# Kernel optimization log

Hardware: AMD Instinct MI355X
Metric: run time of the kernel (lower is better)

Reference implementation:

```python
import jax, jax.numpy as jnp
import numpy as np

N, C, T, V, S = 64, 64, 300, 25, 3  # batch, channels, frames, joints, num_subset
EPS_NORM = 1e-4  # L2_norm epsilon from the torch module
EPS_BN = 1e-5    # torch BatchNorm2d default eps


def setup_inputs() -> dict:
    key = jax.random.key(0)
    ks = jax.random.split(key, 6)
    x = jax.random.normal(ks[0], (N, C, T, V), jnp.float32)
    # adaptive adjacency PA: (num_subset, V, V)
    PA = jax.random.normal(ks[1], (S, V, V), jnp.float32)
    # per-subset 1x1 conv: weight (out_c, in_c), bias (out_c,); conv_branch_init scale
    W = jax.random.normal(ks[2], (S, C, C), jnp.float32) * np.sqrt(2.0 / (C * S)).astype(np.float32)
    b = jax.random.normal(ks[3], (S, C), jnp.float32) * 0.01
    # BatchNorm affine params (training-mode batch stats used in forward)
    gamma = 1.0 + 0.1 * jax.random.normal(ks[4], (C,), jnp.float32)
    beta = 0.1 * jax.random.normal(ks[5], (C,), jnp.float32)
    return {"x": x, "PA": PA, "W": W, "b": b, "gamma": gamma, "beta": beta}


def reference(x, PA, W, b, gamma, beta):
    # L2 normalize adjacency along dim=1 (per subset, per column)
    A = PA / (jnp.linalg.norm(PA, axis=1, keepdims=True) + EPS_NORM)  # (S, V, V)
    # sum over subsets of: graph matmul (nctv,vw->nctw) then 1x1 conv (oc contraction)
    y = jnp.einsum('nctv,svw,soc->notw', x, A, W)
    y = y + b.sum(axis=0)[None, :, None, None]
    # BatchNorm2d in training mode: batch stats over (N, T, V) per channel
    mean = y.mean(axis=(0, 2, 3), keepdims=True)
    var = y.var(axis=(0, 2, 3), keepdims=True)  # biased variance
    y = gamma[None, :, None, None] * (y - mean) * jax.lax.rsqrt(var + EPS_BN) + beta[None, :, None, None]
    # residual (in_c == out_c -> down is identity) + ReLU
    return jax.nn.relu(y + x)
```

## Files before the change

### kernel.cpp

```cpp
#include <hip/hip_runtime.h>
#include <math.h>


typedef __attribute__((ext_vector_type(8))) short bf16x8;
typedef __attribute__((ext_vector_type(4))) float f32x4;
typedef __attribute__((ext_vector_type(4))) ushort u16x4;

__device__ inline ushort f2bf(float f) {
    union { float f; unsigned u; } v; v.f = f;
    unsigned r = v.u + 0x7fffu + ((v.u >> 16) & 1u);
    return (ushort)(r >> 16);
}
__device__ inline float bf2f(ushort h) {
    union { unsigned u; float f; } v; v.u = ((unsigned)h) << 16;
    return v.f;
}

__global__ __launch_bounds__(256) void k_prep(const float* __restrict__ PA,
                                              const float* __restrict__ W,
                                              float* __restrict__ ws) {
    __shared__ float Al[1875];
    const int tid = threadIdx.x;
    const int bid = blockIdx.x;
    for (int i = tid; i < 1875; i += 256) Al[i] = PA[i];
    if (bid == 0)
        for (int i = tid; i < 2048; i += 256) ws[2048 + i] = 0.0f;
    __syncthreads();
    if (tid < 75) {
        int s = tid / 25, w = tid - s * 25;
        float ss = 0.0f;
        for (int v = 0; v < 25; ++v) {
            float p = Al[s * 625 + v * 25 + w];
            ss += p * p;
        }
        float inv = 1.0f / (sqrtf(ss) + 1e-4f);
        for (int v = 0; v < 25; ++v) Al[s * 625 + v * 25 + w] *= inv;
    }
    __syncthreads();
    int idx = bid * 256 + tid;
    if (idx < 1536) {
        ushort* wt = (ushort*)(ws + 4352);
        int lane = idx & 63, rest = idx >> 6;
        int wv = rest & 3, sk = rest >> 2;
        int kt = sk & 1, s = sk >> 1;
        int col = lane & 15, quad = lane >> 4;
        const float* wp = W + s * 4096 + (wv * 16 + col) * 64 + kt * 32 + quad * 8;
#pragma unroll
        for (int j = 0; j < 8; ++j) wt[idx * 8 + j] = f2bf(wp[j]);
    } else if (idx < 1920) {
        ushort* at = (ushort*)(ws + 10496);
        int a = idx - 1536;
        int lane = a & 63, rest = a >> 6;
        int nt2 = rest & 1, s = rest >> 1;
        int col = lane & 15, quad = lane >> 4;
        int w = nt2 * 16 + col;
#pragma unroll
        for (int j = 0; j < 8; ++j) {
            int v = quad * 8 + j;
            float av = (v < 25 && w < 25) ? Al[s * 625 + v * 25 + w] : 0.0f;
            at[a * 8 + j] = f2bf(av);
        }
    }
}

__global__ __launch_bounds__(256, 4) void k_main8(const float* __restrict__ x,
                                                  const float* __restrict__ ws,
                                                  ushort* __restrict__ ypre,
                                                  float* __restrict__ stats) {
    __shared__ __align__(16) ushort Xl[112 * 72];
    __shared__ float sst[128];

    const int tid = threadIdx.x;
    const int wv = tid >> 6;
    const int lane = tid & 63;
    const int col = lane & 15;
    const int quad = lane >> 4;
    const int strip = wv << 4;
    const int n = blockIdx.y;
    const int t0 = blockIdx.x * 4;

    {
        const float* xr = x + n * 480000 + t0 * 25;
        const int c = tid >> 2, part = tid & 3;
        const float4* row = (const float4*)(xr + c * 7500);
        for (int j = part; j < 25; j += 4) {
            float4 v4 = row[j];
            ushort* dst = &Xl[(j * 4) * 72 + c];
            dst[0]   = f2bf(v4.x);
            dst[72]  = f2bf(v4.y);
            dst[144] = f2bf(v4.z);
            dst[216] = f2bf(v4.w);
        }
        for (int i = tid; i < 864; i += 256) Xl[7200 + i] = 0;
    }
    __syncthreads();

    const ushort* wt = (const ushort*)(ws + 4352);
    const ushort* at = (const ushort*)(ws + 10496);

    const int s0l = col + ((quad & 1) << 5);
    const int s1l = s0l + 16;
    const bool hiq = quad >= 2;

    f32x4 yacc[4][2];
#pragma unroll
    for (int t = 0; t < 4; ++t)
#pragma unroll
        for (int j = 0; j < 2; ++j) yacc[t][j] = (f32x4){0.f, 0.f, 0.f, 0.f};

    for (int s = 0; s < 3; ++s) {
        bf16x8 wf0 = *(const bf16x8*)&wt[(((s * 2 + 0) * 4 + wv) * 64 + lane) * 8];
        bf16x8 wf1 = *(const bf16x8*)&wt[(((s * 2 + 1) * 4 + wv) * 64 + lane) * 8];
        bf16x8 af0 = *(const bf16x8*)&at[((s * 2 + 0) * 64 + lane) * 8];
        bf16x8 af1 = *(const bf16x8*)&at[((s * 2 + 1) * 64 + lane) * 8];
#pragma unroll
        for (int t = 0; t < 4; ++t) {
            const int r0 = (t * 25 + col) * 72 + (quad << 3);
            const int r1 = r0 + 16 * 72;
            bf16x8 x00 = *(const bf16x8*)&Xl[r0];
            bf16x8 x01 = *(const bf16x8*)&Xl[r0 + 32];
            bf16x8 x10 = *(const bf16x8*)&Xl[r1];
            bf16x8 x11 = *(const bf16x8*)&Xl[r1 + 32];
            f32x4 zA = (f32x4){0.f, 0.f, 0.f, 0.f};
            f32x4 zB = (f32x4){0.f, 0.f, 0.f, 0.f};
            zA = __builtin_amdgcn_mfma_f32_16x16x32_bf16(x00, wf0, zA, 0, 0, 0);
            zA = __builtin_amdgcn_mfma_f32_16x16x32_bf16(x01, wf1, zA, 0, 0, 0);
            zB = __builtin_amdgcn_mfma_f32_16x16x32_bf16(x10, wf0, zB, 0, 0, 0);
            zB = __builtin_amdgcn_mfma_f32_16x16x32_bf16(x11, wf1, zB, 0, 0, 0);
            unsigned pa0 = (unsigned)f2bf(zA[0]) | ((unsigned)f2bf(zA[1]) << 16);
            unsigned pa1 = (unsigned)f2bf(zA[2]) | ((unsigned)f2bf(zA[3]) << 16);
            unsigned pb0 = (unsigned)f2bf(zB[0]) | ((unsigned)f2bf(zB[1]) << 16);
            unsigned pb1 = (unsigned)f2bf(zB[2]) | ((unsigned)f2bf(zB[3]) << 16);
            unsigned ga0 = __shfl(pa0, s0l);
            unsigned ga1 = __shfl(pa1, s0l);
            unsigned ga2 = __shfl(pa0, s1l);
            unsigned ga3 = __shfl(pa1, s1l);
            unsigned gb0 = __shfl(pb0, s0l);
            unsigned gb1 = __shfl(pb1, s0l);
            unsigned gb2 = __shfl(pb0, s1l);
            unsigned gb3 = __shfl(pb1, s1l);
            union { unsigned u[4]; bf16x8 v; } zf;
            zf.u[0] = hiq ? gb0 : ga0;
            zf.u[1] = hiq ? gb1 : ga1;
            zf.u[2] = hiq ? gb2 : ga2;
            zf.u[3] = hiq ? gb3 : ga3;
            yacc[t][0] = __builtin_amdgcn_mfma_f32_16x16x32_bf16(zf.v, af0, yacc[t][0], 0, 0, 0);
            yacc[t][1] = __builtin_amdgcn_mfma_f32_16x16x32_bf16(zf.v, af1, yacc[t][1], 0, 0, 0);
        }
    }

    float ssum[4] = {0.f, 0.f, 0.f, 0.f}, ssq[4] = {0.f, 0.f, 0.f, 0.f};
    const int obase = strip + (quad << 2);
#pragma unroll
    for (int t = 0; t < 4; ++t)
#pragma unroll
        for (int nt2 = 0; nt2 < 2; ++nt2) {
            int w = nt2 * 16 + col;
            if (w < 25) {
                ushort* yp = ypre + n * 480000 + obase * 7500 + (t0 + t) * 25 + w;
                f32x4 f = yacc[t][nt2];
#pragma unroll
                for (int r = 0; r < 4; ++r) {
                    float yv = f[r];
                    yp[r * 7500] = f2bf(yv);
                    ssum[r] += yv;
                    ssq[r] = fmaf(yv, yv, ssq[r]);
                }
            }
        }
#pragma unroll
    for (int r = 0; r < 4; ++r) {
        float a = ssum[r], b = ssq[r];
        for (int m = 1; m < 16; m <<= 1) {
            a += __shfl_xor(a, m, 64);
            b += __shfl_xor(b, m, 64);
        }
        if (col == 0) {
            sst[obase + r] = a;
            sst[64 + obase + r] = b;
        }
    }
    __syncthreads();
    const int rep = (blockIdx.x + blockIdx.y) & 15;
    if (tid < 128) atomicAdd(&stats[rep * 128 + tid], sst[tid]);
}

__global__ __launch_bounds__(256) void k_bnrelu_c(const float* __restrict__ x,
                                                  const ushort* __restrict__ ypre,
                                                  const float* __restrict__ stats,
                                                  const float* __restrict__ gamma,
                                                  const float* __restrict__ beta,
                                                  float* __restrict__ out) {
    __shared__ float bsc[2];
    const int plane = blockIdx.x;
    const int o = plane & 63;
    const int tid = threadIdx.x;
    if (tid < 16) {
        float su = stats[tid * 128 + o];
        float sq = stats[tid * 128 + 64 + o];
#pragma unroll
        for (int m = 1; m < 16; m <<= 1) {
            su += __shfl_xor(su, m, 64);
            sq += __shfl_xor(sq, m, 64);
        }
        if (tid == 0) {
            const float invn = 1.0f / 480000.0f;
            float mean = su * invn;
            float var = sq * invn - mean * mean;
            float sc = gamma[o] * rsqrtf(var + 1e-5f);
            bsc[0] = sc;
            bsc[1] = beta[o] - mean * sc;
        }
    }
    __syncthreads();
    const float sc = bsc[0], sh = bsc[1];
    const u16x4* yp = (const u16x4*)(ypre + plane * 7500);
    const f32x4* xp = (const f32x4*)(x + plane * 7500);
    f32x4* op = (f32x4*)(out + plane * 7500);
    for (int j = tid; j < 1875; j += 256) {
        u16x4 yv = __builtin_nontemporal_load(&yp[j]);
        f32x4 xx = __builtin_nontemporal_load(&xp[j]);
        f32x4 r;
        r.x = fmaxf(fmaf(bf2f(yv.x), sc, sh) + xx.x, 0.0f);
        r.y = fmaxf(fmaf(bf2f(yv.y), sc, sh) + xx.y, 0.0f);
        r.z = fmaxf(fmaf(bf2f(yv.z), sc, sh) + xx.z, 0.0f);
        r.w = fmaxf(fmaf(bf2f(yv.w), sc, sh) + xx.w, 0.0f);
        __builtin_nontemporal_store(r, &op[j]);
    }
}

extern "C" void kernel_launch(void* const* d_in, const int* in_sizes, int n_in,
                              void* d_out, int out_size, void* d_ws, size_t ws_size,
                              hipStream_t stream) {
    const float* x = (const float*)d_in[0];
    const float* PA = (const float*)d_in[1];
    const float* W = (const float*)d_in[2];
    const float* gamma = (const float*)d_in[4];
    const float* beta = (const float*)d_in[5];
    float* wsf = (float*)d_ws;
    float* out = (float*)d_out;
    ushort* ypre = (ushort*)((char*)d_ws + 65536);

    k_prep<<<8, 256, 0, stream>>>(PA, W, wsf);
    dim3 g(75, 64);
    k_main8<<<g, 256, 0, stream>>>(x, wsf, ypre, wsf + 2048);
    k_bnrelu_c<<<4096, 256, 0, stream>>>(x, ypre, wsf + 2048, gamma, beta, out);
}
```

Before: 317.9 us.

## Stage bf16 pre-BN output in LDS and store it in a block-tiled layout

The main kernel now writes its bf16 results into shared memory (reusing the X tile buffer) and then copies the whole 64x100 tile to global memory with contiguous 16-byte vector stores. Before, each lane issued scattered 2-byte stores with a 7500-element stride. The intermediate buffer layout becomes (n, time-block, channel, 100), so the BN/ReLU kernel must gather 4-element chunks using a divide-by-25 index. The point is to coalesce the write traffic of the intermediate. The cost is an extra barrier, LDS traffic, and less regular reads in the second kernel, which also drops its nontemporal load hints.

```diff
diff --git a/kernel.cpp b/kernel.cpp
--- a/kernel.cpp
+++ b/kernel.cpp
@@ -5,6 +5,7 @@
 typedef __attribute__((ext_vector_type(8))) short bf16x8;
 typedef __attribute__((ext_vector_type(4))) float f32x4;
 typedef __attribute__((ext_vector_type(4))) ushort u16x4;
+typedef __attribute__((ext_vector_type(8))) ushort u16x8;
 
 __device__ inline ushort f2bf(float f) {
     union { float f; unsigned u; } v; v.f = f;
@@ -63,10 +64,10 @@
     }
 }
 
-__global__ __launch_bounds__(256, 4) void k_main8(const float* __restrict__ x,
-                                                  const float* __restrict__ ws,
-                                                  ushort* __restrict__ ypre,
-                                                  float* __restrict__ stats) {
+__global__ __launch_bounds__(256, 4) void k_main11(const float* __restrict__ x,
+                                                   const float* __restrict__ ws,
+                                                   ushort* __restrict__ ypre,
+                                                   float* __restrict__ stats) {
     __shared__ __align__(16) ushort Xl[112 * 72];
     __shared__ float sst[128];
 
@@ -77,7 +78,8 @@
     const int quad = lane >> 4;
     const int strip = wv << 4;
     const int n = blockIdx.y;
-    const int t0 = blockIdx.x * 4;
+    const int bx = blockIdx.x;
+    const int t0 = bx * 4;
 
     {
         const float* xr = x + n * 480000 + t0 * 25;
@@ -149,6 +151,9 @@
         }
     }
 
+    __syncthreads();
+    ushort* Ys = Xl;
+
     float ssum[4] = {0.f, 0.f, 0.f, 0.f}, ssq[4] = {0.f, 0.f, 0.f, 0.f};
     const int obase = strip + (quad << 2);
 #pragma unroll
@@ -157,12 +162,11 @@
         for (int nt2 = 0; nt2 < 2; ++nt2) {
             int w = nt2 * 16 + col;
             if (w < 25) {
-                ushort* yp = ypre + n * 480000 + obase * 7500 + (t0 + t) * 25 + w;
                 f32x4 f = yacc[t][nt2];
 #pragma unroll
                 for (int r = 0; r < 4; ++r) {
                     float yv = f[r];
-                    yp[r * 7500] = f2bf(yv);
+                    Ys[(obase + r) * 100 + t * 25 + w] = f2bf(yv);
                     ssum[r] += yv;
                     ssq[r] = fmaf(yv, yv, ssq[r]);
                 }
@@ -181,11 +185,16 @@
         }
     }
     __syncthreads();
-    const int rep = (blockIdx.x + blockIdx.y) & 15;
+    {
+        u16x8* dst = (u16x8*)(ypre + (size_t)(n * 75 + bx) * 6400);
+        const u16x8* src = (const u16x8*)Ys;
+        for (int i = tid; i < 800; i += 256) dst[i] = src[i];
+    }
+    const int rep = (bx + blockIdx.y) & 15;
     if (tid < 128) atomicAdd(&stats[rep * 128 + tid], sst[tid]);
 }
 
-__global__ __launch_bounds__(256) void k_bnrelu_c(const float* __restrict__ x,
+__global__ __launch_bounds__(256) void k_bnrelu_d(const float* __restrict__ x,
                                                   const ushort* __restrict__ ypre,
                                                   const float* __restrict__ stats,
                                                   const float* __restrict__ gamma,
@@ -194,6 +203,7 @@
     __shared__ float bsc[2];
     const int plane = blockIdx.x;
     const int o = plane & 63;
+    const int n = plane >> 6;
     const int tid = threadIdx.x;
     if (tid < 16) {
         float su = stats[tid * 128 + o];
@@ -214,18 +224,20 @@
     }
     __syncthreads();
     const float sc = bsc[0], sh = bsc[1];
-    const u16x4* yp = (const u16x4*)(ypre + plane * 7500);
-    const f32x4* xp = (const f32x4*)(x + plane * 7500);
-    f32x4* op = (f32x4*)(out + plane * 7500);
-    for (int j = tid; j < 1875; j += 256) {
-        u16x4 yv = __builtin_nontemporal_load(&yp[j]);
-        f32x4 xx = __builtin_nontemporal_load(&xp[j]);
+    const ushort* ybase = ypre + (size_t)n * 480000 + o * 100;
+    const f32x4* xp = (const f32x4*)(x + (size_t)plane * 7500);
+    f32x4* op = (f32x4*)(out + (size_t)plane * 7500);
+    for (int j4 = tid; j4 < 1875; j4 += 256) {
+        int bxi = j4 / 25;
+        int r4 = j4 - bxi * 25;
+        u16x4 yv = *(const u16x4*)(ybase + bxi * 6400 + r4 * 4);
+        f32x4 xx = xp[j4];
         f32x4 r;
         r.x = fmaxf(fmaf(bf2f(yv.x), sc, sh) + xx.x, 0.0f);
         r.y = fmaxf(fmaf(bf2f(yv.y), sc, sh) + xx.y, 0.0f);
         r.z = fmaxf(fmaf(bf2f(yv.z), sc, sh) + xx.z, 0.0f);
         r.w = fmaxf(fmaf(bf2f(yv.w), sc, sh) + xx.w, 0.0f);
-        __builtin_nontemporal_store(r, &op[j]);
+        __builtin_nontemporal_store(r, &op[j4]);
     }
 }
 
@@ -243,6 +255,6 @@
 
     k_prep<<<8, 256, 0, stream>>>(PA, W, wsf);
     dim3 g(75, 64);
-    k_main8<<<g, 256, 0, stream>>>(x, wsf, ypre, wsf + 2048);
-    k_bnrelu_c<<<4096, 256, 0, stream>>>(x, ypre, wsf + 2048, gamma, beta, out);
-}
+    k_main11<<<g, 256, 0, stream>>>(x, wsf, ypre, wsf + 2048);
+    k_bnrelu_d<<<4096, 256, 0, stream>>>(x, ypre, wsf + 2048, gamma, beta, out);
+}
```

New measurement: 310.5 us. -2.3%, faster.
